# Optimization experiments

Measured on AMD Instinct MI355X. Metric: run time of the kernel, lower is better.

## Reference

```python
import jax, jax.numpy as jnp
import numpy as np

B, C, H, W = 16, 512, 32, 32
HID = 4 * C


def setup_inputs() -> dict:
    key = jax.random.key(0)
    k_x, k_w1, k_w2 = jax.random.split(key, 3)
    x = jax.random.normal(k_x, (B, C, H, W), dtype=jnp.float32)
    # 1x1 conv weights stored as [out, in] matrices (kernel_size=1)
    w1 = jax.random.normal(k_w1, (HID, C), dtype=jnp.float32) * (1.0 / np.sqrt(C))
    b1 = jnp.zeros((HID,), dtype=jnp.float32)
    w2 = jax.random.normal(k_w2, (C, HID), dtype=jnp.float32) * (1.0 / np.sqrt(HID))
    b2 = jnp.zeros((C,), dtype=jnp.float32)
    return {"x": x, "w1": w1, "b1": b1, "w2": w2, "b2": b2}


def reference(x, w1, b1, w2, b2):
    Bd, Cd, Hd, Wd = x.shape
    scale = Cd ** (-0.5)
    xf = x.reshape(Bd, Cd, Hd * Wd)          # [B, C, N]
    q = jnp.swapaxes(xf, -1, -2)              # [B, N, C]
    # full spatial self-attention: scores [B, N, N]
    attn = jax.nn.softmax(jnp.einsum('bnc,bcm->bnm', q, xf) * scale, axis=-1)
    out = jnp.einsum('bnm,bmc->bnc', attn, q)  # [B, N, C]
    # 1x1-conv FFN applied per spatial position
    h = jax.nn.relu(jnp.einsum('bnc,dc->bnd', out, w1) + b1)   # [B, N, 4C]
    y = jnp.einsum('bnd,cd->bnc', h, w2) + b2                  # [B, N, C]
    y = jnp.swapaxes(y, -1, -2).reshape(Bd, Cd, Hd, Wd)
    return y + x
```

## Files before the change

### kernel.cpp

```cpp
#include <hip/hip_runtime.h>

#define BATCH 16
#define CH    512
#define NSP   1024
#define HIDD  2048

typedef __bf16 bf16x8 __attribute__((ext_vector_type(8)));
typedef float floatx4 __attribute__((ext_vector_type(4)));

__device__ __forceinline__ float bf2f(unsigned short u) {
    union { unsigned int i; float f; } v; v.i = ((unsigned int)u) << 16; return v.f;
}
__device__ __forceinline__ unsigned short f2bf(float f) {
    union { float f; unsigned int i; } v; v.f = f;
    unsigned int i = v.i;
    return (unsigned short)((i + 0x7FFFu + ((i >> 16) & 1u)) >> 16);
}

__device__ __forceinline__ void gload16(const void* g, void* l) {
    __builtin_amdgcn_global_load_lds(
        (__attribute__((address_space(1))) unsigned int*)(g),
        (__attribute__((address_space(3))) unsigned int*)(l),
        16, 0, 0);
}
#define MEMFENCE asm volatile("" ::: "memory")

template<int EPI, int MAP, int DEPTH>
__global__ __launch_bounds__(256, (DEPTH == 2) ? 3 : 2)
void gemm_bt(const unsigned short* __restrict__ A,
             const unsigned short* __restrict__ Bm,
             void* __restrict__ Cout,
             int Nn, int K,
             long sAb, long sBb, long sCb,
             const float* __restrict__ bias, float scale,
             const float* __restrict__ resid,
             float* __restrict__ aux)
{
    constexpr int NBUF = DEPTH + 1;
    __shared__ unsigned short sA[NBUF][128 * 32];
    __shared__ unsigned short sB[NBUF][128 * 32];

    const int tid  = threadIdx.x;
    const int lane = tid & 63;
    const int w    = tid >> 6;
    const int quad = lane >> 4;
    const int l15  = lane & 15;
    const int mw   = (w >> 1) * 64;
    const int nw   = (w & 1) * 64;

    const int F = blockIdx.x;
    int m0, n0, b;
    if constexpr (MAP == 1) {
        const int xcd = F & 7, s = F >> 3;
        b = xcd + ((s >> 5) << 3);
        const int j = s & 31; m0 = (j >> 2) << 7; n0 = (j & 3) << 7;
    } else if constexpr (MAP == 2) {
        b = 0; m0 = (F >> 4) << 7; n0 = (F & 15) << 7;
    } else if constexpr (MAP == 3) {
        const int xcd = F & 7, s = F >> 3;
        b = 0; m0 = (s & 3) << 7; n0 = ((xcd << 4) + (s >> 2)) << 7;
    } else {
        const int xcd = F & 7; int s = F >> 3;
        b = xcd + ((s >= 36) ? 8 : 0);
        if (s >= 36) s -= 36;
        int tm = 0;
        while (s >= 8 - tm) { s -= 8 - tm; tm++; }
        m0 = tm << 7; n0 = (tm + s) << 7;
    }

    A  += (size_t)b * sAb;
    Bm += (size_t)b * sBb;

    const int srow = lane >> 2;
    const int sg   = (lane & 3) ^ ((lane >> 3) & 3);
    const unsigned short* pA = A  + (size_t)(m0 + w * 32 + srow) * K + sg * 8;
    const unsigned short* pB = Bm + (size_t)(n0 + w * 32 + srow) * K + sg * 8;
    const size_t rowskip16 = (size_t)16 * K;
    const int woff = w * 1024;
    const int rslot = ((l15 >> 1) & 3);

    floatx4 acc[4][4];
#pragma unroll
    for (int i = 0; i < 4; i++)
#pragma unroll
        for (int j = 0; j < 4; j++) acc[i][j] = (floatx4){0.f, 0.f, 0.f, 0.f};

    const int nIter = K >> 5;
    const int kLast = K - 32;

#pragma unroll
    for (int d = 0; d < DEPTH; ++d) {
        unsigned short* dA = &sA[d][0] + woff;
        unsigned short* dB = &sB[d][0] + woff;
        gload16(pA + d * 32,             dA);
        gload16(pA + d * 32 + rowskip16, dA + 512);
        gload16(pB + d * 32,             dB);
        gload16(pB + d * 32 + rowskip16, dB + 512);
        MEMFENCE;
    }

    int bcur = 0, bpf = DEPTH;
    for (int it = 0; it < nIter; ++it) {
        if constexpr (DEPTH == 2)
            asm volatile("s_waitcnt vmcnt(4)\n\ts_barrier" ::: "memory");
        else
            asm volatile("s_waitcnt vmcnt(8)\n\ts_barrier" ::: "memory");

        const int kpf = (it + DEPTH) * 32 <= kLast ? (it + DEPTH) * 32 : kLast;
        unsigned short* dA = &sA[0][0] + bpf * 4096 + woff;
        unsigned short* dB = &sB[0][0] + bpf * 4096 + woff;
        gload16(pA + kpf,             dA);
        gload16(pA + kpf + rowskip16, dA + 512);
        gload16(pB + kpf,             dB);
        gload16(pB + kpf + rowskip16, dB + 512);
        MEMFENCE;

        const unsigned short* bufA = &sA[0][0] + bcur * 4096;
        const unsigned short* bufB = &sB[0][0] + bcur * 4096;
        bf16x8 af[4], bfr[4];
#pragma unroll
        for (int mi = 0; mi < 4; mi++)
            af[mi] = *(const bf16x8*)(bufA + (mw + mi * 16 + l15) * 32
                                      + (quad ^ rslot) * 8);
#pragma unroll
        for (int ni = 0; ni < 4; ni++)
            bfr[ni] = *(const bf16x8*)(bufB + (nw + ni * 16 + l15) * 32
                                       + (quad ^ rslot) * 8);
#pragma unroll
        for (int mi = 0; mi < 4; mi++)
#pragma unroll
            for (int ni = 0; ni < 4; ni++)
                acc[mi][ni] = __builtin_amdgcn_mfma_f32_16x16x32_bf16(
                    af[mi], bfr[ni], acc[mi][ni], 0, 0, 0);

        bcur = bcur == NBUF - 1 ? 0 : bcur + 1;
        bpf  = bpf  == NBUF - 1 ? 0 : bpf  + 1;
    }
    asm volatile("s_waitcnt vmcnt(0)" ::: "memory");

    if constexpr (EPI == 4) {
        float* Of = (float*)Cout;
#pragma unroll
        for (int mi = 0; mi < 4; mi++) {
#pragma unroll
            for (int r = 0; r < 4; r++) {
                const int c = m0 + mw + mi * 16 + quad * 4 + r;
                const float bv = bias[c];
#pragma unroll
                for (int ni = 0; ni < 4; ni++) {
                    const int j  = n0 + nw + ni * 16 + l15;
                    const int bb = j >> 10, ns = j & 1023;
                    const size_t a = (size_t)bb * CH * NSP + (size_t)c * NSP + ns;
                    Of[a] = acc[mi][ni][r] + bv + resid[a];
                }
            }
        }
    } else if constexpr (EPI == 5) {
#pragma unroll
        for (int mi = 0; mi < 4; mi++)
#pragma unroll
            for (int ni = 0; ni < 4; ni++)
#pragma unroll
                for (int r = 0; r < 4; r++)
                    acc[mi][ni][r] = __expf(acc[mi][ni][r] * scale);
        {
            const int chunk = (n0 + nw) >> 6;
            float* ps = aux + (size_t)b * NSP * 16;
#pragma unroll
            for (int mi = 0; mi < 4; mi++) {
#pragma unroll
                for (int r = 0; r < 4; r++) {
                    float s = acc[mi][0][r] + acc[mi][1][r]
                            + acc[mi][2][r] + acc[mi][3][r];
                    s += __shfl_xor(s, 1);
                    s += __shfl_xor(s, 2);
                    s += __shfl_xor(s, 4);
                    s += __shfl_xor(s, 8);
                    if (l15 == 0)
                        ps[(size_t)(m0 + mw + mi * 16 + quad * 4 + r) * 16
                           + chunk] = s;
                }
            }
        }
        unsigned short* Cb = (unsigned short*)Cout + (size_t)b * sCb;
#pragma unroll
        for (int mi = 0; mi < 4; mi++) {
#pragma unroll
            for (int r = 0; r < 4; r++) {
                const size_t rowoff =
                    (size_t)(m0 + mw + mi * 16 + quad * 4 + r) * Nn;
#pragma unroll
                for (int ni = 0; ni < 4; ni++)
                    Cb[rowoff + n0 + nw + ni * 16 + l15] =
                        f2bf(acc[mi][ni][r]);
            }
        }
        if constexpr (MAP == 4) {
            if (m0 != n0) {
                const int chunkt = (m0 + mw) >> 6;
                float* ps = aux + (size_t)b * NSP * 16;
#pragma unroll
                for (int ni = 0; ni < 4; ni++) {
                    float s = 0.f;
#pragma unroll
                    for (int mi = 0; mi < 4; mi++)
#pragma unroll
                        for (int r = 0; r < 4; r++) s += acc[mi][ni][r];
                    s += __shfl_xor(s, 16);
                    s += __shfl_xor(s, 32);
                    if (quad == 0)
                        ps[(size_t)(n0 + nw + ni * 16 + l15) * 16 + chunkt] = s;
                }
#pragma unroll
                for (int ni = 0; ni < 4; ni++) {
                    const size_t rowoff =
                        (size_t)(n0 + nw + ni * 16 + l15) * Nn;
#pragma unroll
                    for (int mi = 0; mi < 4; mi++) {
                        ushort4 v;
                        v.x = f2bf(acc[mi][ni][0]);
                        v.y = f2bf(acc[mi][ni][1]);
                        v.z = f2bf(acc[mi][ni][2]);
                        v.w = f2bf(acc[mi][ni][3]);
                        *(ushort4*)(Cb + rowoff + m0 + mw + mi * 16 + quad * 4)
                            = v;
                    }
                }
            }
        }
    } else if constexpr (EPI == 6) {
        const float* invp = aux + (size_t)b * NSP;
        unsigned short* Cb = (unsigned short*)Cout + (size_t)b * sCb;
#pragma unroll
        for (int mi = 0; mi < 4; mi++) {
#pragma unroll
            for (int r = 0; r < 4; r++) {
                const int row = m0 + mw + mi * 16 + quad * 4 + r;
                const float iv = invp[row];
                const size_t rowoff = (size_t)row * Nn;
#pragma unroll
                for (int ni = 0; ni < 4; ni++)
                    Cb[rowoff + n0 + nw + ni * 16 + l15] =
                        f2bf(acc[mi][ni][r] * iv);
            }
        }
    } else {
        unsigned short* Cb = (unsigned short*)Cout + (size_t)b * sCb;
        float bv[4];
#pragma unroll
        for (int ni = 0; ni < 4; ni++) bv[ni] = bias[n0 + nw + ni * 16 + l15];
#pragma unroll
        for (int mi = 0; mi < 4; mi++) {
#pragma unroll
            for (int r = 0; r < 4; r++) {
                const size_t rowoff =
                    (size_t)(m0 + mw + mi * 16 + quad * 4 + r) * Nn;
#pragma unroll
                for (int ni = 0; ni < 4; ni++)
                    Cb[rowoff + n0 + nw + ni * 16 + l15] =
                        f2bf(fmaxf(acc[mi][ni][r] + bv[ni], 0.f));
            }
        }
    }
}

__global__ __launch_bounds__(256)
void rowsum_inv_kernel(const float* __restrict__ ps, float* __restrict__ inv)
{
    const int i = blockIdx.x * 256 + threadIdx.x;
    const float* p = ps + (size_t)i * 16;
    float s = 0.f;
#pragma unroll
    for (int k = 0; k < 16; k++) s += p[k];
    inv[i] = 1.0f / s;
}

__global__ __launch_bounds__(256)
void pack_x_kernel(const float* __restrict__ x,
                   unsigned short* __restrict__ Xbf,
                   unsigned short* __restrict__ XT)
{
    __shared__ float tile[32][33];
    const int tx = threadIdx.x, ty = threadIdx.y;
    const int n0 = blockIdx.x * 32, c0 = blockIdx.y * 32, b = blockIdx.z;
    const size_t base = (size_t)b * CH * NSP;
#pragma unroll
    for (int i = ty; i < 32; i += 8) {
        float v = x[base + (size_t)(c0 + i) * NSP + n0 + tx];
        tile[i][tx] = v;
        Xbf[base + (size_t)(c0 + i) * NSP + n0 + tx] = f2bf(v);
    }
    __syncthreads();
    const size_t tbase = (size_t)b * NSP * CH;
#pragma unroll
    for (int i = ty; i < 32; i += 8)
        XT[tbase + (size_t)(n0 + i) * CH + c0 + tx] = f2bf(tile[tx][i]);
}

__global__ __launch_bounds__(256)
void cast_bf16_kernel(const float* __restrict__ src,
                      unsigned short* __restrict__ dst, int n)
{
    int i = blockIdx.x * 256 + threadIdx.x;
    if (i < n) dst[i] = f2bf(src[i]);
}

extern "C" void kernel_launch(void* const* d_in, const int* in_sizes, int n_in,
                              void* d_out, int out_size, void* d_ws, size_t ws_size,
                              hipStream_t stream)
{
    const float* x  = (const float*)d_in[0];
    const float* w1 = (const float*)d_in[1];
    const float* b1 = (const float*)d_in[2];
    const float* w2 = (const float*)d_in[3];
    const float* b2 = (const float*)d_in[4];
    float* out = (float*)d_out;

    char* ws = (char*)d_ws;
    unsigned short* Xbf = (unsigned short*)ws; ws += (size_t)BATCH * CH * NSP * 2;
    unsigned short* XT  = (unsigned short*)ws; ws += (size_t)BATCH * NSP * CH * 2;
    unsigned short* W1b = (unsigned short*)ws; ws += (size_t)HIDD * CH * 2;
    unsigned short* W2b = (unsigned short*)ws; ws += (size_t)CH * HIDD * 2;
    unsigned short* P   = (unsigned short*)ws; ws += (size_t)BATCH * NSP * NSP * 2;
    unsigned short* O   = (unsigned short*)ws; ws += (size_t)BATCH * NSP * CH * 2;
    unsigned short* Hb  = (unsigned short*)ws; ws += (size_t)BATCH * NSP * HIDD * 2;
    float*          Ps  = (float*)ws;          ws += (size_t)BATCH * NSP * 16 * 4;
    float*          Inv = (float*)ws;          ws += (size_t)BATCH * NSP * 4;

    const dim3 blk(256);

    pack_x_kernel<<<dim3(NSP / 32, CH / 32, BATCH), dim3(32, 8), 0, stream>>>(x, Xbf, XT);
    cast_bf16_kernel<<<dim3((HIDD * CH) / 256), blk, 0, stream>>>(w1, W1b, HIDD * CH);
    cast_bf16_kernel<<<dim3((CH * HIDD) / 256), blk, 0, stream>>>(w2, W2b, CH * HIDD);

    gemm_bt<5, 4, 2><<<dim3(576), blk, 0, stream>>>(
        XT, XT, P, NSP, CH,
        (long)NSP * CH, (long)NSP * CH, (long)NSP * NSP, nullptr,
        0.04419417382415922f, nullptr, Ps);

    rowsum_inv_kernel<<<dim3(BATCH * NSP / 256), blk, 0, stream>>>(Ps, Inv);

    gemm_bt<6, 1, 2><<<dim3(512), blk, 0, stream>>>(
        P, Xbf, O, CH, NSP,
        (long)NSP * NSP, (long)CH * NSP, (long)NSP * CH, nullptr, 1.f,
        nullptr, Inv);

    gemm_bt<2, 2, 2><<<dim3(2048), blk, 0, stream>>>(
        O, W1b, Hb, HIDD, CH, 0, 0, 0, b1, 1.f, nullptr, nullptr);

    gemm_bt<4, 3, 3><<<dim3(512), blk, 0, stream>>>(
        W2b, Hb, out, BATCH * NSP, HIDD, 0, 0, 0, b2, 1.f, x, nullptr);
}
```

Before: 262.7 us.

## Fuse prep kernels, fold rowsum into PV GEMM, add wide FFN1 tile

Merges the x pack/transpose and both weight casts into a single prep launch. Drops the separate rowsum-inverse kernel: the PV GEMM now sums the partial row sums into shared memory itself. Replaces the 128x128 FFN1 GEMM with a dedicated 128x256 tile kernel with triple-buffered LDS loads, which raises operand reuse per block. The cost is extra LDS and register pressure in the wide kernel and a few redundant partial-sum reads per PV block.

```diff
diff --git a/kernel.cpp b/kernel.cpp
--- a/kernel.cpp
+++ b/kernel.cpp
@@ -39,6 +39,7 @@
     constexpr int NBUF = DEPTH + 1;
     __shared__ unsigned short sA[NBUF][128 * 32];
     __shared__ unsigned short sB[NBUF][128 * 32];
+    __shared__ float sInv[128];
 
     const int tid  = threadIdx.x;
     const int lane = tid & 63;
@@ -54,8 +55,6 @@
         const int xcd = F & 7, s = F >> 3;
         b = xcd + ((s >> 5) << 3);
         const int j = s & 31; m0 = (j >> 2) << 7; n0 = (j & 3) << 7;
-    } else if constexpr (MAP == 2) {
-        b = 0; m0 = (F >> 4) << 7; n0 = (F & 15) << 7;
     } else if constexpr (MAP == 3) {
         const int xcd = F & 7, s = F >> 3;
         b = 0; m0 = (s & 3) << 7; n0 = ((xcd << 4) + (s >> 2)) << 7;
@@ -66,6 +65,18 @@
         int tm = 0;
         while (s >= 8 - tm) { s -= 8 - tm; tm++; }
         m0 = tm << 7; n0 = (tm + s) << 7;
+    }
+
+    if constexpr (EPI == 6) {
+        if (tid < 128) {
+            const float* p = aux + (size_t)b * NSP * 16
+                           + (size_t)(m0 + tid) * 16;
+            float s = 0.f;
+#pragma unroll
+            for (int k = 0; k < 16; k++) s += p[k];
+            sInv[tid] = 1.0f / s;
+        }
+        MEMFENCE;
     }
 
     A  += (size_t)b * sAb;
@@ -228,81 +239,166 @@
                 }
             }
         }
-    } else if constexpr (EPI == 6) {
-        const float* invp = aux + (size_t)b * NSP;
+    } else {
+        __syncthreads();
         unsigned short* Cb = (unsigned short*)Cout + (size_t)b * sCb;
 #pragma unroll
         for (int mi = 0; mi < 4; mi++) {
 #pragma unroll
             for (int r = 0; r < 4; r++) {
-                const int row = m0 + mw + mi * 16 + quad * 4 + r;
-                const float iv = invp[row];
-                const size_t rowoff = (size_t)row * Nn;
+                const int lrow = mw + mi * 16 + quad * 4 + r;
+                const float iv = sInv[lrow];
+                const size_t rowoff = (size_t)(m0 + lrow) * Nn;
 #pragma unroll
                 for (int ni = 0; ni < 4; ni++)
                     Cb[rowoff + n0 + nw + ni * 16 + l15] =
                         f2bf(acc[mi][ni][r] * iv);
             }
         }
+    }
+}
+
+__global__ __launch_bounds__(256, 2)
+void ffn1_wide(const unsigned short* __restrict__ A,
+               const unsigned short* __restrict__ Bm,
+               unsigned short* __restrict__ Cout,
+               const float* __restrict__ bias)
+{
+    const int K = CH, Nn = HIDD;
+    __shared__ unsigned short sA[3][128 * 32];
+    __shared__ unsigned short sB[3][256 * 32];
+
+    const int tid  = threadIdx.x;
+    const int lane = tid & 63;
+    const int w    = tid >> 6;
+    const int quad = lane >> 4;
+    const int l15  = lane & 15;
+    const int mw   = (w >> 1) * 64;
+    const int nw   = (w & 1) * 128;
+
+    const int F = blockIdx.x;
+    const int m0 = (F >> 3) << 7;
+    const int n0 = (F & 7) << 8;
+
+    const int srow = lane >> 2;
+    const int sg   = (lane & 3) ^ ((lane >> 3) & 3);
+    const unsigned short* pA = A  + (size_t)(m0 + w * 32 + srow) * K + sg * 8;
+    const unsigned short* pB = Bm + (size_t)(n0 + w * 64 + srow) * K + sg * 8;
+    const size_t rowskip16 = (size_t)16 * K;
+    const int woffA = w * 1024;
+    const int woffB = w * 2048;
+    const int rslot = ((l15 >> 1) & 3);
+
+    floatx4 acc[4][8];
+#pragma unroll
+    for (int i = 0; i < 4; i++)
+#pragma unroll
+        for (int j = 0; j < 8; j++) acc[i][j] = (floatx4){0.f, 0.f, 0.f, 0.f};
+
+    const int nIter = K >> 5;
+    const int kLast = K - 32;
+
+#pragma unroll
+    for (int d = 0; d < 2; ++d) {
+        unsigned short* dA = &sA[d][0] + woffA;
+        unsigned short* dB = &sB[d][0] + woffB;
+        gload16(pA + d * 32,                 dA);
+        gload16(pA + d * 32 +     rowskip16, dA + 512);
+        gload16(pB + d * 32,                 dB);
+        gload16(pB + d * 32 +     rowskip16, dB + 512);
+        gload16(pB + d * 32 + 2 * rowskip16, dB + 1024);
+        gload16(pB + d * 32 + 3 * rowskip16, dB + 1536);
+        MEMFENCE;
+    }
+
+    int bcur = 0, bpf = 2;
+    for (int it = 0; it < nIter; ++it) {
+        asm volatile("s_waitcnt vmcnt(6)\n\ts_barrier" ::: "memory");
+
+        const int kpf = (it + 2) * 32 <= kLast ? (it + 2) * 32 : kLast;
+        unsigned short* dA = &sA[0][0] + bpf * 4096 + woffA;
+        unsigned short* dB = &sB[0][0] + bpf * 8192 + woffB;
+        gload16(pA + kpf,                 dA);
+        gload16(pA + kpf +     rowskip16, dA + 512);
+        gload16(pB + kpf,                 dB);
+        gload16(pB + kpf +     rowskip16, dB + 512);
+        gload16(pB + kpf + 2 * rowskip16, dB + 1024);
+        gload16(pB + kpf + 3 * rowskip16, dB + 1536);
+        MEMFENCE;
+
+        const unsigned short* bufA = &sA[0][0] + bcur * 4096;
+        const unsigned short* bufB = &sB[0][0] + bcur * 8192;
+        bf16x8 af[4], bfr[8];
+#pragma unroll
+        for (int mi = 0; mi < 4; mi++)
+            af[mi] = *(const bf16x8*)(bufA + (mw + mi * 16 + l15) * 32
+                                      + (quad ^ rslot) * 8);
+#pragma unroll
+        for (int ni = 0; ni < 8; ni++)
+            bfr[ni] = *(const bf16x8*)(bufB + (nw + ni * 16 + l15) * 32
+                                       + (quad ^ rslot) * 8);
+#pragma unroll
+        for (int mi = 0; mi < 4; mi++)
+#pragma unroll
+            for (int ni = 0; ni < 8; ni++)
+                acc[mi][ni] = __builtin_amdgcn_mfma_f32_16x16x32_bf16(
+                    af[mi], bfr[ni], acc[mi][ni], 0, 0, 0);
+
+        bcur = bcur == 2 ? 0 : bcur + 1;
+        bpf  = bpf  == 2 ? 0 : bpf  + 1;
+    }
+    asm volatile("s_waitcnt vmcnt(0)" ::: "memory");
+
+    float bv[8];
+#pragma unroll
+    for (int ni = 0; ni < 8; ni++) bv[ni] = bias[n0 + nw + ni * 16 + l15];
+#pragma unroll
+    for (int mi = 0; mi < 4; mi++) {
+#pragma unroll
+        for (int r = 0; r < 4; r++) {
+            const size_t rowoff =
+                (size_t)(m0 + mw + mi * 16 + quad * 4 + r) * Nn;
+#pragma unroll
+            for (int ni = 0; ni < 8; ni++)
+                Cout[rowoff + n0 + nw + ni * 16 + l15] =
+                    f2bf(fmaxf(acc[mi][ni][r] + bv[ni], 0.f));
+        }
+    }
+}
+
+__global__ __launch_bounds__(256)
+void prep_kernel(const float* __restrict__ x,
+                 unsigned short* __restrict__ Xbf,
+                 unsigned short* __restrict__ XT,
+                 const float* __restrict__ w1,
+                 unsigned short* __restrict__ W1b,
+                 const float* __restrict__ w2,
+                 unsigned short* __restrict__ W2b)
+{
+    const int tx = threadIdx.x, ty = threadIdx.y;
+    const int z = blockIdx.z;
+    if (z < 16) {
+        __shared__ float tile[32][33];
+        const int n0 = blockIdx.x * 32, c0 = blockIdx.y * 32, b = z;
+        const size_t base = (size_t)b * CH * NSP;
+#pragma unroll
+        for (int i = ty; i < 32; i += 8) {
+            float v = x[base + (size_t)(c0 + i) * NSP + n0 + tx];
+            tile[i][tx] = v;
+            Xbf[base + (size_t)(c0 + i) * NSP + n0 + tx] = f2bf(v);
+        }
+        __syncthreads();
+        const size_t tbase = (size_t)b * NSP * CH;
+#pragma unroll
+        for (int i = ty; i < 32; i += 8)
+            XT[tbase + (size_t)(n0 + i) * CH + c0 + tx] = f2bf(tile[tx][i]);
     } else {
-        unsigned short* Cb = (unsigned short*)Cout + (size_t)b * sCb;
-        float bv[4];
-#pragma unroll
-        for (int ni = 0; ni < 4; ni++) bv[ni] = bias[n0 + nw + ni * 16 + l15];
-#pragma unroll
-        for (int mi = 0; mi < 4; mi++) {
-#pragma unroll
-            for (int r = 0; r < 4; r++) {
-                const size_t rowoff =
-                    (size_t)(m0 + mw + mi * 16 + quad * 4 + r) * Nn;
-#pragma unroll
-                for (int ni = 0; ni < 4; ni++)
-                    Cb[rowoff + n0 + nw + ni * 16 + l15] =
-                        f2bf(fmaxf(acc[mi][ni][r] + bv[ni], 0.f));
-            }
-        }
-    }
-}
-
-__global__ __launch_bounds__(256)
-void rowsum_inv_kernel(const float* __restrict__ ps, float* __restrict__ inv)
-{
-    const int i = blockIdx.x * 256 + threadIdx.x;
-    const float* p = ps + (size_t)i * 16;
-    float s = 0.f;
-#pragma unroll
-    for (int k = 0; k < 16; k++) s += p[k];
-    inv[i] = 1.0f / s;
-}
-
-__global__ __launch_bounds__(256)
-void pack_x_kernel(const float* __restrict__ x,
-                   unsigned short* __restrict__ Xbf,
-                   unsigned short* __restrict__ XT)
-{
-    __shared__ float tile[32][33];
-    const int tx = threadIdx.x, ty = threadIdx.y;
-    const int n0 = blockIdx.x * 32, c0 = blockIdx.y * 32, b = blockIdx.z;
-    const size_t base = (size_t)b * CH * NSP;
-#pragma unroll
-    for (int i = ty; i < 32; i += 8) {
-        float v = x[base + (size_t)(c0 + i) * NSP + n0 + tx];
-        tile[i][tx] = v;
-        Xbf[base + (size_t)(c0 + i) * NSP + n0 + tx] = f2bf(v);
-    }
-    __syncthreads();
-    const size_t tbase = (size_t)b * NSP * CH;
-#pragma unroll
-    for (int i = ty; i < 32; i += 8)
-        XT[tbase + (size_t)(n0 + i) * CH + c0 + tx] = f2bf(tile[tx][i]);
-}
-
-__global__ __launch_bounds__(256)
-void cast_bf16_kernel(const float* __restrict__ src,
-                      unsigned short* __restrict__ dst, int n)
-{
-    int i = blockIdx.x * 256 + threadIdx.x;
-    if (i < n) dst[i] = f2bf(src[i]);
+        const int tid = ty * 32 + tx;
+        const int blk = (z - 16) * 512 + blockIdx.y * 32 + blockIdx.x;
+        const int i = blk * 256 + tid;
+        if (i < HIDD * CH) W1b[i] = f2bf(w1[i]);
+        else               W2b[i - HIDD * CH] = f2bf(w2[i - HIDD * CH]);
+    }
 }
 
 extern "C" void kernel_launch(void* const* d_in, const int* in_sizes, int n_in,
@@ -325,28 +421,23 @@
     unsigned short* O   = (unsigned short*)ws; ws += (size_t)BATCH * NSP * CH * 2;
     unsigned short* Hb  = (unsigned short*)ws; ws += (size_t)BATCH * NSP * HIDD * 2;
     float*          Ps  = (float*)ws;          ws += (size_t)BATCH * NSP * 16 * 4;
-    float*          Inv = (float*)ws;          ws += (size_t)BATCH * NSP * 4;
 
     const dim3 blk(256);
 
-    pack_x_kernel<<<dim3(NSP / 32, CH / 32, BATCH), dim3(32, 8), 0, stream>>>(x, Xbf, XT);
-    cast_bf16_kernel<<<dim3((HIDD * CH) / 256), blk, 0, stream>>>(w1, W1b, HIDD * CH);
-    cast_bf16_kernel<<<dim3((CH * HIDD) / 256), blk, 0, stream>>>(w2, W2b, CH * HIDD);
+    prep_kernel<<<dim3(32, 16, 32), dim3(32, 8), 0, stream>>>(
+        x, Xbf, XT, w1, W1b, w2, W2b);
 
     gemm_bt<5, 4, 2><<<dim3(576), blk, 0, stream>>>(
         XT, XT, P, NSP, CH,
         (long)NSP * CH, (long)NSP * CH, (long)NSP * NSP, nullptr,
         0.04419417382415922f, nullptr, Ps);
 
-    rowsum_inv_kernel<<<dim3(BATCH * NSP / 256), blk, 0, stream>>>(Ps, Inv);
-
     gemm_bt<6, 1, 2><<<dim3(512), blk, 0, stream>>>(
         P, Xbf, O, CH, NSP,
         (long)NSP * NSP, (long)CH * NSP, (long)NSP * CH, nullptr, 1.f,
-        nullptr, Inv);
-
-    gemm_bt<2, 2, 2><<<dim3(2048), blk, 0, stream>>>(
-        O, W1b, Hb, HIDD, CH, 0, 0, 0, b1, 1.f, nullptr, nullptr);
+        nullptr, Ps);
+
+    ffn1_wide<<<dim3(1024), blk, 0, stream>>>(O, W1b, Hb, b1);
 
     gemm_bt<4, 3, 3><<<dim3(512), blk, 0, stream>>>(
         W2b, Hb, out, BATCH * NSP, HIDD, 0, 0, 0, b2, 1.f, x, nullptr);
```

Result: no change. 258.4 us (-1.6%).
